# Kernel tuning notes

Measured on AMD Instinct MI355X. Metric: run time of the kernel, lower is better.

## Reference

```python
import jax, jax.numpy as jnp
import numpy as np

DIM = 2048
NUM_LADDERS = 3
DEPTH = 5
EPS = 0.01


def setup_inputs() -> dict:
    key = jax.random.key(0)
    ks = jax.random.split(key, 5)
    s = 1.0 / np.sqrt(DIM)
    x = jax.random.normal(ks[0], (4, 2048, DIM), dtype=jnp.float32)
    U_w = jax.random.uniform(ks[1], (DIM, DIM), jnp.float32, -s, s)          # U.weight  [out,in]
    gate_w = jax.random.uniform(ks[2], (DIM, DIM), jnp.float32, -s, s)       # gate_proj.weight
    ladder_w = jax.random.uniform(ks[3], (NUM_LADDERS, DEPTH + 1, DIM), jnp.float32, -s, s)
    V_w = jax.random.uniform(ks[4], (DIM, NUM_LADDERS), jnp.float32, -1.0 / np.sqrt(NUM_LADDERS), 1.0 / np.sqrt(NUM_LADDERS))
    return {"x": x, "U_w": U_w, "gate_w": gate_w, "ladder_w": ladder_w, "V_w": V_w}


def _continued_fraction(a_cf, eps):
    # a_cf: (..., depth). Evaluate a_1/(1 + a_2/(1 + ... a_d/1)) with
    # epsilon-guarded denominators (pole avoidance).
    d = a_cf.shape[-1]
    f = jnp.zeros(a_cf.shape[:-1], a_cf.dtype)
    for k in reversed(range(d)):  # tiny fixed depth: loop is fine
        denom = 1.0 + f
        denom = jnp.where(jnp.abs(denom) < eps,
                          jnp.where(denom >= 0, eps, -eps), denom)
        f = a_cf[..., k] / denom
    return f


def reference(x, U_w, gate_w, ladder_w, V_w):
    linear_out = jnp.einsum('bsd,od->bso', x, U_w)                 # U(x)
    gated_x = jax.nn.sigmoid(jnp.einsum('bsd,od->bso', x, gate_w)) * x
    # All ladders at once: (b,s,L,depth+1)
    a = jnp.einsum('bsd,lkd->bslk', gated_x, ladder_w)
    a0 = a[..., 0]                                                 # (b,s,L)
    z = a0 + _continued_fraction(a[..., 1:], EPS)                  # (b,s,L)
    combined = jnp.einsum('bsl,dl->bsd', z, V_w)                   # V(z)
    return linear_out + combined
```

## Files before the change

### kernel.cpp

```cpp
#include <hip/hip_runtime.h>
#include <cstdint>
#include <cstddef>

#define DIM 2048
#define NROWS 8192
#define NL 3
#define DEPTH 5
#define NLK 18
#define NCB 16
#define CF_EPS 0.01f

typedef __attribute__((ext_vector_type(8))) __bf16 bfrag;
typedef __attribute__((ext_vector_type(4))) float f32x4;

typedef __attribute__((address_space(1))) void gvoid;
typedef __attribute__((address_space(3))) void lvoid;

__device__ __forceinline__ void gld_lds16(const void* g, void* l) {
    __builtin_amdgcn_global_load_lds((gvoid*)g, (lvoid*)l, 16, 0, 0);
}

__global__ __launch_bounds__(256) void mfma_gemm_u(
    const ushort* __restrict__ A, const ushort* __restrict__ B,
    const float* __restrict__ zb, const float* __restrict__ Vp,
    float* __restrict__ C)
{
    constexpr int BK = 32;
    constexpr int SUB = 128 * BK;
    __shared__ __align__(16) ushort sA[2 * SUB];
    __shared__ __align__(16) ushort sB[2 * SUB];

    const int tid  = threadIdx.x;
    const int wave = tid >> 6;
    const int lane = tid & 63;
    const int wm   = wave & 1;
    const int wn   = wave >> 1;
    const int m0   = blockIdx.y * 128;
    const int n0   = blockIdx.x * 128;

    const size_t soff = (size_t)(wave * 32 + (lane >> 2)) * DIM + (lane & 3) * 8;
    const ushort* gA = A + (size_t)m0 * DIM + soff;
    const ushort* gB = B + (size_t)n0 * DIM + soff;

    ushort* lA0 = &sA[(wave * 32) * BK];
    ushort* lA1 = &sA[(wave * 32 + 16) * BK];
    ushort* lB0 = &sB[(wave * 32) * BK];
    ushort* lB1 = &sB[(wave * 32 + 16) * BK];

    const int fm = lane & 15;
    const int fq = lane >> 4;

    f32x4 acc[4][4];
    #pragma unroll
    for (int i = 0; i < 4; ++i)
        #pragma unroll
        for (int j = 0; j < 4; ++j)
            acc[i][j] = (f32x4){0.f, 0.f, 0.f, 0.f};

    for (int k0 = 0; k0 < DIM; k0 += 2 * BK) {
        __syncthreads();
        gld_lds16(gA + k0, lA0);
        gld_lds16(gA + (size_t)16 * DIM + k0, lA1);
        gld_lds16(gB + k0, lB0);
        gld_lds16(gB + (size_t)16 * DIM + k0, lB1);
        gld_lds16(gA + k0 + BK, lA0 + SUB);
        gld_lds16(gA + (size_t)16 * DIM + k0 + BK, lA1 + SUB);
        gld_lds16(gB + k0 + BK, lB0 + SUB);
        gld_lds16(gB + (size_t)16 * DIM + k0 + BK, lB1 + SUB);
        __syncthreads();

        #pragma unroll
        for (int ks = 0; ks < 2; ++ks) {
            const ushort* pA = &sA[ks * SUB];
            const ushort* pB = &sB[ks * SUB];
            bfrag ah[4], bh[4];
            #pragma unroll
            for (int i = 0; i < 4; ++i) {
                ah[i] = *(const bfrag*)&pA[(wm * 64 + i * 16 + fm) * BK + fq * 8];
                bh[i] = *(const bfrag*)&pB[(wn * 64 + i * 16 + fm) * BK + fq * 8];
            }
            #pragma unroll
            for (int i = 0; i < 4; ++i)
                #pragma unroll
                for (int j = 0; j < 4; ++j)
                    acc[i][j] = __builtin_amdgcn_mfma_f32_16x16x32_bf16(ah[i], bh[j], acc[i][j], 0, 0, 0);
        }
    }

    float4 vc[4];
    #pragma unroll
    for (int j = 0; j < 4; ++j)
        vc[j] = *(const float4*)&Vp[(size_t)(n0 + wn * 64 + j * 16 + fm) * 4];

    #pragma unroll
    for (int i = 0; i < 4; ++i) {
        const int rowb = m0 + wm * 64 + i * 16 + fq * 4;
        #pragma unroll
        for (int r = 0; r < 4; ++r) {
            const float4 zr = *(const float4*)&zb[(size_t)(rowb + r) * 4];
            #pragma unroll
            for (int j = 0; j < 4; ++j) {
                const int col = n0 + wn * 64 + j * 16 + fm;
                C[(size_t)(rowb + r) * DIM + col] =
                    acc[i][j][r] + zr.x * vc[j].x + zr.y * vc[j].y + zr.z * vc[j].z;
            }
        }
    }
}

__global__ __launch_bounds__(256) void mfma_gemm_gate(
    const ushort* __restrict__ Ah, const ushort* __restrict__ Al,
    const ushort* __restrict__ Bh, const ushort* __restrict__ Bl,
    const float* __restrict__ X,  const float* __restrict__ Lw,
    float* __restrict__ a_part)
{
    constexpr int BK = 32;
    __shared__ __align__(16) char smem[32768];
    ushort* sAh = (ushort*)(smem);
    ushort* sBh = (ushort*)(smem + 8192);
    ushort* sAl = (ushort*)(smem + 16384);
    ushort* sBl = (ushort*)(smem + 24576);
    float*  sG  = (float*)(smem);
    float*  sLw = (float*)(smem + 16896);

    const int tid  = threadIdx.x;
    const int wave = tid >> 6;
    const int lane = tid & 63;
    const int wm   = wave & 1;
    const int wn   = wave >> 1;
    const int m0   = blockIdx.y * 128;
    const int n0   = blockIdx.x * 128;

    const size_t soff = (size_t)(wave * 32 + (lane >> 2)) * DIM + (lane & 3) * 8;
    const ushort* gA  = Ah + (size_t)m0 * DIM + soff;
    const ushort* gAl = Al + (size_t)m0 * DIM + soff;
    const ushort* gB  = Bh + (size_t)n0 * DIM + soff;
    const ushort* gBl = Bl + (size_t)n0 * DIM + soff;

    ushort* lA0  = &sAh[(wave * 32) * BK];
    ushort* lA1  = &sAh[(wave * 32 + 16) * BK];
    ushort* lB0  = &sBh[(wave * 32) * BK];
    ushort* lB1  = &sBh[(wave * 32 + 16) * BK];
    ushort* lAl0 = &sAl[(wave * 32) * BK];
    ushort* lAl1 = &sAl[(wave * 32 + 16) * BK];
    ushort* lBl0 = &sBl[(wave * 32) * BK];
    ushort* lBl1 = &sBl[(wave * 32 + 16) * BK];

    const int fm = lane & 15;
    const int fq = lane >> 4;

    f32x4 acc[4][4];
    #pragma unroll
    for (int i = 0; i < 4; ++i)
        #pragma unroll
        for (int j = 0; j < 4; ++j)
            acc[i][j] = (f32x4){0.f, 0.f, 0.f, 0.f};

    for (int k0 = 0; k0 < DIM; k0 += BK) {
        __syncthreads();
        gld_lds16(gA + k0, lA0);
        gld_lds16(gA + (size_t)16 * DIM + k0, lA1);
        gld_lds16(gB + k0, lB0);
        gld_lds16(gB + (size_t)16 * DIM + k0, lB1);
        gld_lds16(gAl + k0, lAl0);
        gld_lds16(gAl + (size_t)16 * DIM + k0, lAl1);
        gld_lds16(gBl + k0, lBl0);
        gld_lds16(gBl + (size_t)16 * DIM + k0, lBl1);
        __syncthreads();

        bfrag ah[4], bh[4], al[4], bl[4];
        #pragma unroll
        for (int i = 0; i < 4; ++i) {
            ah[i] = *(const bfrag*)&sAh[(wm * 64 + i * 16 + fm) * BK + fq * 8];
            bh[i] = *(const bfrag*)&sBh[(wn * 64 + i * 16 + fm) * BK + fq * 8];
            al[i] = *(const bfrag*)&sAl[(wm * 64 + i * 16 + fm) * BK + fq * 8];
            bl[i] = *(const bfrag*)&sBl[(wn * 64 + i * 16 + fm) * BK + fq * 8];
        }
        #pragma unroll
        for (int i = 0; i < 4; ++i)
            #pragma unroll
            for (int j = 0; j < 4; ++j) {
                acc[i][j] = __builtin_amdgcn_mfma_f32_16x16x32_bf16(ah[i], bh[j], acc[i][j], 0, 0, 0);
                acc[i][j] = __builtin_amdgcn_mfma_f32_16x16x32_bf16(ah[i], bl[j], acc[i][j], 0, 0, 0);
                acc[i][j] = __builtin_amdgcn_mfma_f32_16x16x32_bf16(al[i], bh[j], acc[i][j], 0, 0, 0);
            }
    }

    const float* xblk = X + (size_t)m0 * DIM + n0;
    const int rred  = ((tid >> 6) << 3) | (tid & 7);
    const int strip = (lane >> 3) & 7;
    const int qc    = strip * 16;

#define DO_QUARTER(Q)                                                          \
    {                                                                          \
        __syncthreads();     \
        if (Q == 0) {                                                          \
              \
            for (int idx = tid; idx < NLK * 128; idx += 256) {                 \
                const int lk = idx >> 7, c = idx & 127;                        \
                sLw[lk * 156 + c + ((c >> 4) << 2)] = Lw[(size_t)lk * DIM + n0 + c]; \
            }                                                                  \
        }                                                                      \
        if (wm == (Q >> 1)) {                                                  \
            constexpr int ib = (Q & 1) * 2;   \
            _Pragma("unroll")                                                  \
            for (int ii = 0; ii < 2; ++ii) {                                   \
                _Pragma("unroll")                                              \
                for (int r = 0; r < 4; ++r) {                                  \
                    const int rloc = ii * 16 + fq * 4 + r;          \
                    const float* xr = xblk + (size_t)(Q * 32 + rloc) * DIM;    \
                    _Pragma("unroll")                                          \
                    for (int j = 0; j < 4; ++j) {                              \
                        const int cc = wn * 64 + j * 16 + fm;                  \
                        const float g = acc[ib + ii][j][r];                    \
                        const float s = 1.0f / (1.0f + __expf(-g));            \
                        sG[rloc * 132 + cc] = s * xr[cc];                      \
                    }                                                          \
                }                                                              \
            }                                                                  \
        }                                                                      \
        __syncthreads();                         \
        float p[NLK];                                                          \
        _Pragma("unroll")                                                      \
        for (int lk = 0; lk < NLK; ++lk) p[lk] = 0.f;                          \
        _Pragma("unroll")                                                      \
        for (int c4 = 0; c4 < 16; c4 += 4) {                                   \
            const float4 g4 = *(const float4*)&sG[rred * 132 + qc + c4];       \
            _Pragma("unroll")                                                  \
            for (int lk = 0; lk < NLK; ++lk) {                                 \
                const float4 w4 = *(const float4*)&sLw[lk * 156 + qc + c4 + (strip << 2)]; \
                p[lk] = fmaf(g4.x, w4.x, fmaf(g4.y, w4.y,                      \
                        fmaf(g4.z, w4.z, fmaf(g4.w, w4.w, p[lk]))));           \
            }                                                                  \
        }                                                                      \
        _Pragma("unroll")                                                      \
        for (int lk = 0; lk < NLK; ++lk) {                                     \
            p[lk] += __shfl_xor(p[lk], 8, 64);                                 \
            p[lk] += __shfl_xor(p[lk], 16, 64);                                \
            p[lk] += __shfl_xor(p[lk], 32, 64);                                \
        }                                                                      \
        if ((lane >> 3) == 0) {                                                \
            float* dst = a_part +                                              \
                ((size_t)(m0 + Q * 32 + rred) * NCB + blockIdx.x) * NLK;       \
            _Pragma("unroll")                                                  \
            for (int lk = 0; lk < NLK; ++lk) dst[lk] = p[lk];                  \
        }                                                                      \
    }

    DO_QUARTER(0)
    DO_QUARTER(1)
    DO_QUARTER(2)
    DO_QUARTER(3)
#undef DO_QUARTER
}

__global__ __launch_bounds__(256) void cf_kernel(const float* __restrict__ a_part,
                                                 float* __restrict__ zb)
{
    const int r = blockIdx.x * 256 + threadIdx.x;
    const float* ap = a_part + (size_t)r * NCB * NLK;
    float a[NLK];
    #pragma unroll
    for (int lk = 0; lk < NLK; ++lk) a[lk] = 0.f;
    #pragma unroll 4
    for (int cb = 0; cb < NCB; ++cb) {
        #pragma unroll
        for (int lk = 0; lk < NLK; ++lk)
            a[lk] += ap[cb * NLK + lk];
    }
    float z[NL];
    #pragma unroll
    for (int l = 0; l < NL; ++l) {
        float f = 0.f;
        #pragma unroll
        for (int k = DEPTH - 1; k >= 0; --k) {
            float denom = 1.f + f;
            if (fabsf(denom) < CF_EPS) denom = (denom >= 0.f) ? CF_EPS : -CF_EPS;
            f = a[l * (DEPTH + 1) + k + 1] / denom;
        }
        z[l] = a[l * (DEPTH + 1)] + f;
    }
    *(float4*)&zb[(size_t)r * 4] = make_float4(z[0], z[1], z[2], 0.f);
}

__global__ __launch_bounds__(256) void padV(const float* __restrict__ Vw,
                                            float* __restrict__ Vp)
{
    const int d = blockIdx.x * 256 + threadIdx.x;
    *(float4*)&Vp[(size_t)d * 4] =
        make_float4(Vw[(size_t)d * 3], Vw[(size_t)d * 3 + 1], Vw[(size_t)d * 3 + 2], 0.f);
}

__device__ __forceinline__ ushort f2bf_bits(float f) {
    __bf16 h = (__bf16)f;
    return __builtin_bit_cast(unsigned short, h);
}
__device__ __forceinline__ float bfbits2f(ushort u) {
    __bf16 h = __builtin_bit_cast(__bf16, u);
    return (float)h;
}

union U16x8 { ushort u[8]; uint4 v; };

__global__ __launch_bounds__(256) void split2(const float* __restrict__ src,
                                              ushort* __restrict__ hi,
                                              ushort* __restrict__ lo)
{
    const size_t i0 = ((size_t)blockIdx.x * 256 + threadIdx.x) * 8;
    const float4 v0 = *(const float4*)(src + i0);
    const float4 v1 = *(const float4*)(src + i0 + 4);
    const float f[8] = {v0.x, v0.y, v0.z, v0.w, v1.x, v1.y, v1.z, v1.w};
    U16x8 h, l;
    #pragma unroll
    for (int j = 0; j < 8; ++j) {
        const ushort hb = f2bf_bits(f[j]);
        h.u[j] = hb;
        l.u[j] = f2bf_bits(f[j] - bfbits2f(hb));
    }
    *(uint4*)(hi + i0) = h.v;
    *(uint4*)(lo + i0) = l.v;
}

__global__ __launch_bounds__(256) void tobf16(const float* __restrict__ src,
                                              ushort* __restrict__ dst)
{
    const size_t i0 = ((size_t)blockIdx.x * 256 + threadIdx.x) * 8;
    const float4 v0 = *(const float4*)(src + i0);
    const float4 v1 = *(const float4*)(src + i0 + 4);
    const float f[8] = {v0.x, v0.y, v0.z, v0.w, v1.x, v1.y, v1.z, v1.w};
    U16x8 h;
    #pragma unroll
    for (int j = 0; j < 8; ++j) h.u[j] = f2bf_bits(f[j]);
    *(uint4*)(dst + i0) = h.v;
}

#define BMF 128
#define BNF 128
#define BKF 16
#define LDAF 132

__global__ __launch_bounds__(256) void sgemm_dual(
    const float* __restrict__ X,
    const float* __restrict__ Uw,
    const float* __restrict__ Gw,
    float* __restrict__ outLin,
    float* __restrict__ outGate)
{
    __shared__ float As[BKF][LDAF];
    __shared__ float Bs[BKF][LDAF];

    const int tid = threadIdx.x;
    const int n0 = blockIdx.x * BNF;
    const int m0 = blockIdx.y * BMF;
    const bool isGate = (n0 >= DIM);
    const float* W = isGate ? Gw : Uw;
    float* C = isGate ? outGate : outLin;
    const int nb = isGate ? (n0 - DIM) : n0;

    const int lr = tid >> 2;
    const int lc = (tid & 3) << 2;

    const float* pa0 = X + (size_t)(m0 + lr) * DIM + lc;
    const float* pa1 = X + (size_t)(m0 + lr + 64) * DIM + lc;
    const float* pb0 = W + (size_t)(nb + lr) * DIM + lc;
    const float* pb1 = W + (size_t)(nb + lr + 64) * DIM + lc;

    const int tx = tid & 15;
    const int ty = tid >> 4;

    float acc[8][8];
    #pragma unroll
    for (int i = 0; i < 8; ++i)
        #pragma unroll
        for (int j = 0; j < 8; ++j) acc[i][j] = 0.f;

    for (int k0 = 0; k0 < DIM; k0 += BKF) {
        const float4 a0 = *(const float4*)(pa0 + k0);
        const float4 a1 = *(const float4*)(pa1 + k0);
        const float4 b0 = *(const float4*)(pb0 + k0);
        const float4 b1 = *(const float4*)(pb1 + k0);
        __syncthreads();
        As[lc + 0][lr] = a0.x; As[lc + 1][lr] = a0.y; As[lc + 2][lr] = a0.z; As[lc + 3][lr] = a0.w;
        As[lc + 0][lr + 64] = a1.x; As[lc + 1][lr + 64] = a1.y; As[lc + 2][lr + 64] = a1.z; As[lc + 3][lr + 64] = a1.w;
        Bs[lc + 0][lr] = b0.x; Bs[lc + 1][lr] = b0.y; Bs[lc + 2][lr] = b0.z; Bs[lc + 3][lr] = b0.w;
        Bs[lc + 0][lr + 64] = b1.x; Bs[lc + 1][lr + 64] = b1.y; Bs[lc + 2][lr + 64] = b1.z; Bs[lc + 3][lr + 64] = b1.w;
        __syncthreads();
        #pragma unroll
        for (int kk = 0; kk < BKF; ++kk) {
            float av[8], bv[8];
            *(float4*)&av[0] = *(const float4*)&As[kk][ty * 8];
            *(float4*)&av[4] = *(const float4*)&As[kk][ty * 8 + 4];
            *(float4*)&bv[0] = *(const float4*)&Bs[kk][tx * 8];
            *(float4*)&bv[4] = *(const float4*)&Bs[kk][tx * 8 + 4];
            #pragma unroll
            for (int i = 0; i < 8; ++i)
                #pragma unroll
                for (int j = 0; j < 8; ++j)
                    acc[i][j] = fmaf(av[i], bv[j], acc[i][j]);
        }
    }

    #pragma unroll
    for (int i = 0; i < 8; ++i) {
        float* crow = C + (size_t)(m0 + ty * 8 + i) * DIM + nb + tx * 8;
        *(float4*)crow       = make_float4(acc[i][0], acc[i][1], acc[i][2], acc[i][3]);
        *(float4*)(crow + 4) = make_float4(acc[i][4], acc[i][5], acc[i][6], acc[i][7]);
    }
}

__global__ __launch_bounds__(256) void ladder_epilogue(
    const float* __restrict__ X,
    const float* __restrict__ G,
    const float* __restrict__ Lw,
    const float* __restrict__ Vw,
    float* __restrict__ Out)
{
    const int r = blockIdx.x;
    const int tid = threadIdx.x;
    const int d0 = tid * 8;
    const float* xrow = X + (size_t)r * DIM;
    const float* grow = G + (size_t)r * DIM;

    const float4 xv0 = *(const float4*)(xrow + d0);
    const float4 xv1 = *(const float4*)(xrow + d0 + 4);
    const float4 gv0 = *(const float4*)(grow + d0);
    const float4 gv1 = *(const float4*)(grow + d0 + 4);

    float gated[8];
    {
        const float gx[8] = {gv0.x, gv0.y, gv0.z, gv0.w, gv1.x, gv1.y, gv1.z, gv1.w};
        const float xx[8] = {xv0.x, xv0.y, xv0.z, xv0.w, xv1.x, xv1.y, xv1.z, xv1.w};
        #pragma unroll
        for (int j = 0; j < 8; ++j) {
            const float s = 1.0f / (1.0f + __expf(-gx[j]));
            gated[j] = s * xx[j];
        }
    }

    float part[NLK];
    #pragma unroll
    for (int lk = 0; lk < NLK; ++lk) {
        const float* lrow = Lw + (size_t)lk * DIM + d0;
        const float4 w0 = *(const float4*)lrow;
        const float4 w1 = *(const float4*)(lrow + 4);
        part[lk] = gated[0] * w0.x + gated[1] * w0.y + gated[2] * w0.z + gated[3] * w0.w
                 + gated[4] * w1.x + gated[5] * w1.y + gated[6] * w1.z + gated[7] * w1.w;
    }

    #pragma unroll
    for (int off = 32; off > 0; off >>= 1) {
        #pragma unroll
        for (int lk = 0; lk < NLK; ++lk)
            part[lk] += __shfl_down(part[lk], off, 64);
    }

    __shared__ float red[4][NLK];
    __shared__ float zsh[NL];
    const int wave = tid >> 6;
    const int lane = tid & 63;
    if (lane == 0) {
        #pragma unroll
        for (int lk = 0; lk < NLK; ++lk) red[wave][lk] = part[lk];
    }
    __syncthreads();
    if (tid < NL) {
        float a[DEPTH + 1];
        #pragma unroll
        for (int k = 0; k < DEPTH + 1; ++k)
            a[k] = red[0][tid * 6 + k] + red[1][tid * 6 + k]
                 + red[2][tid * 6 + k] + red[3][tid * 6 + k];
        float f = 0.f;
        #pragma unroll
        for (int k = DEPTH - 1; k >= 0; --k) {
            float denom = 1.f + f;
            if (fabsf(denom) < CF_EPS) denom = (denom >= 0.f) ? CF_EPS : -CF_EPS;
            f = a[k + 1] / denom;
        }
        zsh[tid] = a[0] + f;
    }
    __syncthreads();
    const float z0 = zsh[0], z1 = zsh[1], z2 = zsh[2];

    float* orow = Out + (size_t)r * DIM + d0;
    const float4 o0 = *(const float4*)orow;
    const float4 o1 = *(const float4*)(orow + 4);
    float ov[8] = {o0.x, o0.y, o0.z, o0.w, o1.x, o1.y, o1.z, o1.w};
    #pragma unroll
    for (int j = 0; j < 8; ++j) {
        const float* vp = Vw + (size_t)(d0 + j) * NL;
        ov[j] += z0 * vp[0] + z1 * vp[1] + z2 * vp[2];
    }
    *(float4*)orow       = make_float4(ov[0], ov[1], ov[2], ov[3]);
    *(float4*)(orow + 4) = make_float4(ov[4], ov[5], ov[6], ov[7]);
}

extern "C" void kernel_launch(void* const* d_in, const int* in_sizes, int n_in,
                              void* d_out, int out_size, void* d_ws, size_t ws_size,
                              hipStream_t stream) {
    const float* X  = (const float*)d_in[0];
    const float* Uw = (const float*)d_in[1];
    const float* Gw = (const float*)d_in[2];
    const float* Lw = (const float*)d_in[3];
    const float* Vw = (const float*)d_in[4];
    float* out = (float*)d_out;

    const size_t WS_NEED = 101875712ull;
    char* ws = (char*)d_ws;

    if (ws_size >= WS_NEED) {
        ushort* Xh     = (ushort*)(ws);
        ushort* Xl     = (ushort*)(ws + 33554432);
        ushort* Gwh    = (ushort*)(ws + 67108864);
        ushort* Gwl    = (ushort*)(ws + 75497472);
        ushort* Uwh    = (ushort*)(ws + 83886080);
        float*  a_part = (float*)(ws + 92274688);
        float*  z_buf  = (float*)(ws + 101711872);
        float*  Vp     = (float*)(ws + 101842944);

        split2<<<dim3(8192), dim3(256), 0, stream>>>(X, Xh, Xl);
        split2<<<dim3(2048), dim3(256), 0, stream>>>(Gw, Gwh, Gwl);
        tobf16<<<dim3(2048), dim3(256), 0, stream>>>(Uw, Uwh);
        padV  <<<dim3(8),    dim3(256), 0, stream>>>(Vw, Vp);

        dim3 grid(DIM / 128, NROWS / 128);
        mfma_gemm_gate<<<grid, dim3(256), 0, stream>>>(Xh, Xl, Gwh, Gwl, X, Lw, a_part);
        cf_kernel<<<dim3(32), dim3(256), 0, stream>>>(a_part, z_buf);
        mfma_gemm_u<<<grid, dim3(256), 0, stream>>>(Xh, Uwh, z_buf, Vp, out);
    } else {
        float* gbuf = (float*)ws;
        dim3 grid(2 * DIM / BNF, NROWS / BMF);
        sgemm_dual<<<grid, dim3(256), 0, stream>>>(X, Uw, Gw, out, gbuf);
        ladder_epilogue<<<dim3(NROWS), dim3(256), 0, stream>>>(X, gbuf, Lw, Vw, out);
    }
}
```

Baseline: 485.6 us.

## Merge gate and U GEMMs into one launch; apply CF and V in a final row pass

The gate GEMM (with its ladder epilogue) and the U GEMM now run as one kernel, with odd and even block columns selecting which GEMM each block computes. This lets both run concurrently and cuts a launch plus the serialization between them. The continued-fraction reduction and the V(z) rank-3 update move into a new per-row kernel that reads back the full output, adds z·V, and writes it again. That costs an extra read and write of the 64MB output, and the interleaved blocks have unequal work, since gate blocks do split-precision loads while U blocks do a single bf16 pass.

```diff
diff --git a/kernel.cpp b/kernel.cpp
--- a/kernel.cpp
+++ b/kernel.cpp
@@ -20,102 +20,95 @@
     __builtin_amdgcn_global_load_lds((gvoid*)g, (lvoid*)l, 16, 0, 0);
 }
 
-__global__ __launch_bounds__(256) void mfma_gemm_u(
-    const ushort* __restrict__ A, const ushort* __restrict__ B,
-    const float* __restrict__ zb, const float* __restrict__ Vp,
-    float* __restrict__ C)
+__global__ __launch_bounds__(256) void gemm_mixed(
+    const ushort* __restrict__ Xh, const ushort* __restrict__ Xl,
+    const ushort* __restrict__ Gwh, const ushort* __restrict__ Gwl,
+    const ushort* __restrict__ Uwh,
+    const float* __restrict__ X,  const float* __restrict__ Lw,
+    float* __restrict__ outU, float* __restrict__ a_part)
 {
     constexpr int BK = 32;
-    constexpr int SUB = 128 * BK;
-    __shared__ __align__(16) ushort sA[2 * SUB];
-    __shared__ __align__(16) ushort sB[2 * SUB];
+    __shared__ __align__(16) char smem[32768];
 
     const int tid  = threadIdx.x;
     const int wave = tid >> 6;
     const int lane = tid & 63;
     const int wm   = wave & 1;
     const int wn   = wave >> 1;
+    const int bx   = blockIdx.x;
+    const int cb   = bx >> 1;
     const int m0   = blockIdx.y * 128;
-    const int n0   = blockIdx.x * 128;
-
-    const size_t soff = (size_t)(wave * 32 + (lane >> 2)) * DIM + (lane & 3) * 8;
-    const ushort* gA = A + (size_t)m0 * DIM + soff;
-    const ushort* gB = B + (size_t)n0 * DIM + soff;
-
-    ushort* lA0 = &sA[(wave * 32) * BK];
-    ushort* lA1 = &sA[(wave * 32 + 16) * BK];
-    ushort* lB0 = &sB[(wave * 32) * BK];
-    ushort* lB1 = &sB[(wave * 32 + 16) * BK];
+    const int n0   = cb * 128;
 
     const int fm = lane & 15;
     const int fq = lane >> 4;
 
-    f32x4 acc[4][4];
-    #pragma unroll
-    for (int i = 0; i < 4; ++i)
-        #pragma unroll
-        for (int j = 0; j < 4; ++j)
-            acc[i][j] = (f32x4){0.f, 0.f, 0.f, 0.f};
-
-    for (int k0 = 0; k0 < DIM; k0 += 2 * BK) {
-        __syncthreads();
-        gld_lds16(gA + k0, lA0);
-        gld_lds16(gA + (size_t)16 * DIM + k0, lA1);
-        gld_lds16(gB + k0, lB0);
-        gld_lds16(gB + (size_t)16 * DIM + k0, lB1);
-        gld_lds16(gA + k0 + BK, lA0 + SUB);
-        gld_lds16(gA + (size_t)16 * DIM + k0 + BK, lA1 + SUB);
-        gld_lds16(gB + k0 + BK, lB0 + SUB);
-        gld_lds16(gB + (size_t)16 * DIM + k0 + BK, lB1 + SUB);
-        __syncthreads();
-
-        #pragma unroll
-        for (int ks = 0; ks < 2; ++ks) {
-            const ushort* pA = &sA[ks * SUB];
-            const ushort* pB = &sB[ks * SUB];
-            bfrag ah[4], bh[4];
+    const size_t soff = (size_t)(wave * 32 + (lane >> 2)) * DIM + (lane & 3) * 8;
+
+    if (bx & 1) {
+        constexpr int SUB = 128 * BK;
+        ushort* sA = (ushort*)smem;
+        ushort* sB = (ushort*)(smem + 16384);
+
+        const ushort* gA = Xh  + (size_t)m0 * DIM + soff;
+        const ushort* gB = Uwh + (size_t)n0 * DIM + soff;
+
+        ushort* lA0 = &sA[(wave * 32) * BK];
+        ushort* lA1 = &sA[(wave * 32 + 16) * BK];
+        ushort* lB0 = &sB[(wave * 32) * BK];
+        ushort* lB1 = &sB[(wave * 32 + 16) * BK];
+
+        f32x4 acc[4][4];
+        #pragma unroll
+        for (int i = 0; i < 4; ++i)
             #pragma unroll
-            for (int i = 0; i < 4; ++i) {
-                ah[i] = *(const bfrag*)&pA[(wm * 64 + i * 16 + fm) * BK + fq * 8];
-                bh[i] = *(const bfrag*)&pB[(wn * 64 + i * 16 + fm) * BK + fq * 8];
+            for (int j = 0; j < 4; ++j)
+                acc[i][j] = (f32x4){0.f, 0.f, 0.f, 0.f};
+
+        for (int k0 = 0; k0 < DIM; k0 += 2 * BK) {
+            __syncthreads();
+            gld_lds16(gA + k0, lA0);
+            gld_lds16(gA + (size_t)16 * DIM + k0, lA1);
+            gld_lds16(gB + k0, lB0);
+            gld_lds16(gB + (size_t)16 * DIM + k0, lB1);
+            gld_lds16(gA + k0 + BK, lA0 + SUB);
+            gld_lds16(gA + (size_t)16 * DIM + k0 + BK, lA1 + SUB);
+            gld_lds16(gB + k0 + BK, lB0 + SUB);
+            gld_lds16(gB + (size_t)16 * DIM + k0 + BK, lB1 + SUB);
+            __syncthreads();
+
+            #pragma unroll
+            for (int ks = 0; ks < 2; ++ks) {
+                const ushort* pA = &sA[ks * SUB];
+                const ushort* pB = &sB[ks * SUB];
+                bfrag ah[4], bh[4];
+                #pragma unroll
+                for (int i = 0; i < 4; ++i) {
+                    ah[i] = *(const bfrag*)&pA[(wm * 64 + i * 16 + fm) * BK + fq * 8];
+                    bh[i] = *(const bfrag*)&pB[(wn * 64 + i * 16 + fm) * BK + fq * 8];
+                }
+                #pragma unroll
+                for (int i = 0; i < 4; ++i)
+                    #pragma unroll
+                    for (int j = 0; j < 4; ++j)
+                        acc[i][j] = __builtin_amdgcn_mfma_f32_16x16x32_bf16(ah[i], bh[j], acc[i][j], 0, 0, 0);
             }
-            #pragma unroll
-            for (int i = 0; i < 4; ++i)
-                #pragma unroll
-                for (int j = 0; j < 4; ++j)
-                    acc[i][j] = __builtin_amdgcn_mfma_f32_16x16x32_bf16(ah[i], bh[j], acc[i][j], 0, 0, 0);
-        }
-    }
-
-    float4 vc[4];
-    #pragma unroll
-    for (int j = 0; j < 4; ++j)
-        vc[j] = *(const float4*)&Vp[(size_t)(n0 + wn * 64 + j * 16 + fm) * 4];
-
-    #pragma unroll
-    for (int i = 0; i < 4; ++i) {
-        const int rowb = m0 + wm * 64 + i * 16 + fq * 4;
-        #pragma unroll
-        for (int r = 0; r < 4; ++r) {
-            const float4 zr = *(const float4*)&zb[(size_t)(rowb + r) * 4];
+        }
+
+        #pragma unroll
+        for (int i = 0; i < 4; ++i) {
+            const int rowb = m0 + wm * 64 + i * 16 + fq * 4;
             #pragma unroll
             for (int j = 0; j < 4; ++j) {
                 const int col = n0 + wn * 64 + j * 16 + fm;
-                C[(size_t)(rowb + r) * DIM + col] =
-                    acc[i][j][r] + zr.x * vc[j].x + zr.y * vc[j].y + zr.z * vc[j].z;
+                #pragma unroll
+                for (int r = 0; r < 4; ++r)
+                    outU[(size_t)(rowb + r) * DIM + col] = acc[i][j][r];
             }
         }
-    }
-}
-
-__global__ __launch_bounds__(256) void mfma_gemm_gate(
-    const ushort* __restrict__ Ah, const ushort* __restrict__ Al,
-    const ushort* __restrict__ Bh, const ushort* __restrict__ Bl,
-    const float* __restrict__ X,  const float* __restrict__ Lw,
-    float* __restrict__ a_part)
-{
-    constexpr int BK = 32;
-    __shared__ __align__(16) char smem[32768];
+        return;
+    }
+
     ushort* sAh = (ushort*)(smem);
     ushort* sBh = (ushort*)(smem + 8192);
     ushort* sAl = (ushort*)(smem + 16384);
@@ -123,19 +116,10 @@
     float*  sG  = (float*)(smem);
     float*  sLw = (float*)(smem + 16896);
 
-    const int tid  = threadIdx.x;
-    const int wave = tid >> 6;
-    const int lane = tid & 63;
-    const int wm   = wave & 1;
-    const int wn   = wave >> 1;
-    const int m0   = blockIdx.y * 128;
-    const int n0   = blockIdx.x * 128;
-
-    const size_t soff = (size_t)(wave * 32 + (lane >> 2)) * DIM + (lane & 3) * 8;
-    const ushort* gA  = Ah + (size_t)m0 * DIM + soff;
-    const ushort* gAl = Al + (size_t)m0 * DIM + soff;
-    const ushort* gB  = Bh + (size_t)n0 * DIM + soff;
-    const ushort* gBl = Bl + (size_t)n0 * DIM + soff;
+    const ushort* gA  = Xh  + (size_t)m0 * DIM + soff;
+    const ushort* gAl = Xl  + (size_t)m0 * DIM + soff;
+    const ushort* gB  = Gwh + (size_t)n0 * DIM + soff;
+    const ushort* gBl = Gwl + (size_t)n0 * DIM + soff;
 
     ushort* lA0  = &sAh[(wave * 32) * BK];
     ushort* lA1  = &sAh[(wave * 32 + 16) * BK];
@@ -145,9 +129,6 @@
     ushort* lAl1 = &sAl[(wave * 32 + 16) * BK];
     ushort* lBl0 = &sBl[(wave * 32) * BK];
     ushort* lBl1 = &sBl[(wave * 32 + 16) * BK];
-
-    const int fm = lane & 15;
-    const int fq = lane >> 4;
 
     f32x4 acc[4][4];
     #pragma unroll
@@ -241,7 +222,7 @@
         }                                                                      \
         if ((lane >> 3) == 0) {                                                \
             float* dst = a_part +                                              \
-                ((size_t)(m0 + Q * 32 + rred) * NCB + blockIdx.x) * NLK;       \
+                ((size_t)(m0 + Q * 32 + rred) * NCB + cb) * NLK;               \
             _Pragma("unroll")                                                  \
             for (int lk = 0; lk < NLK; ++lk) dst[lk] = p[lk];                  \
         }                                                                      \
@@ -254,33 +235,48 @@
 #undef DO_QUARTER
 }
 
-__global__ __launch_bounds__(256) void cf_kernel(const float* __restrict__ a_part,
-                                                 float* __restrict__ zb)
-{
-    const int r = blockIdx.x * 256 + threadIdx.x;
-    const float* ap = a_part + (size_t)r * NCB * NLK;
-    float a[NLK];
-    #pragma unroll
-    for (int lk = 0; lk < NLK; ++lk) a[lk] = 0.f;
-    #pragma unroll 4
-    for (int cb = 0; cb < NCB; ++cb) {
-        #pragma unroll
-        for (int lk = 0; lk < NLK; ++lk)
-            a[lk] += ap[cb * NLK + lk];
-    }
-    float z[NL];
-    #pragma unroll
-    for (int l = 0; l < NL; ++l) {
+__global__ __launch_bounds__(256) void zv_cf_add(
+    float* __restrict__ out, const float* __restrict__ a_part,
+    const float* __restrict__ Vp)
+{
+    __shared__ float red[NLK];
+    __shared__ float zsh[NL];
+    const int r = blockIdx.x;
+    const int tid = threadIdx.x;
+
+    if (tid < NLK) {
+        const float* ap = a_part + (size_t)r * NCB * NLK + tid;
+        float s = 0.f;
+        #pragma unroll
+        for (int cb = 0; cb < NCB; ++cb) s += ap[cb * NLK];
+        red[tid] = s;
+    }
+    __syncthreads();
+    if (tid < NL) {
         float f = 0.f;
         #pragma unroll
         for (int k = DEPTH - 1; k >= 0; --k) {
             float denom = 1.f + f;
             if (fabsf(denom) < CF_EPS) denom = (denom >= 0.f) ? CF_EPS : -CF_EPS;
-            f = a[l * (DEPTH + 1) + k + 1] / denom;
-        }
-        z[l] = a[l * (DEPTH + 1)] + f;
-    }
-    *(float4*)&zb[(size_t)r * 4] = make_float4(z[0], z[1], z[2], 0.f);
+            f = red[tid * 6 + k + 1] / denom;
+        }
+        zsh[tid] = red[tid * 6] + f;
+    }
+    __syncthreads();
+    const float z0 = zsh[0], z1 = zsh[1], z2 = zsh[2];
+
+    const int c0 = tid * 8;
+    float* orow = out + (size_t)r * DIM + c0;
+    const float4 o0 = *(const float4*)orow;
+    const float4 o1 = *(const float4*)(orow + 4);
+    float ov[8] = {o0.x, o0.y, o0.z, o0.w, o1.x, o1.y, o1.z, o1.w};
+    #pragma unroll
+    for (int j = 0; j < 8; ++j) {
+        const float4 v = *(const float4*)&Vp[(size_t)(c0 + j) * 4];
+        ov[j] += z0 * v.x + z1 * v.y + z2 * v.z;
+    }
+    *(float4*)orow       = make_float4(ov[0], ov[1], ov[2], ov[3]);
+    *(float4*)(orow + 4) = make_float4(ov[4], ov[5], ov[6], ov[7]);
 }
 
 __global__ __launch_bounds__(256) void padV(const float* __restrict__ Vw,
@@ -504,7 +500,7 @@
     const float* Vw = (const float*)d_in[4];
     float* out = (float*)d_out;
 
-    const size_t WS_NEED = 101875712ull;
+    const size_t WS_NEED = 101744640ull;
     char* ws = (char*)d_ws;
 
     if (ws_size >= WS_NEED) {
@@ -514,18 +510,16 @@
         ushort* Gwl    = (ushort*)(ws + 75497472);
         ushort* Uwh    = (ushort*)(ws + 83886080);
         float*  a_part = (float*)(ws + 92274688);
-        float*  z_buf  = (float*)(ws + 101711872);
-        float*  Vp     = (float*)(ws + 101842944);
+        float*  Vp     = (float*)(ws + 101711872);
 
         split2<<<dim3(8192), dim3(256), 0, stream>>>(X, Xh, Xl);
         split2<<<dim3(2048), dim3(256), 0, stream>>>(Gw, Gwh, Gwl);
         tobf16<<<dim3(2048), dim3(256), 0, stream>>>(Uw, Uwh);
         padV  <<<dim3(8),    dim3(256), 0, stream>>>(Vw, Vp);
 
-        dim3 grid(DIM / 128, NROWS / 128);
-        mfma_gemm_gate<<<grid, dim3(256), 0, stream>>>(Xh, Xl, Gwh, Gwl, X, Lw, a_part);
-        cf_kernel<<<dim3(32), dim3(256), 0, stream>>>(a_part, z_buf);
-        mfma_gemm_u<<<grid, dim3(256), 0, stream>>>(Xh, Uwh, z_buf, Vp, out);
+        gemm_mixed<<<dim3(32, 64), dim3(256), 0, stream>>>(Xh, Xl, Gwh, Gwl, Uwh,
+                                                           X, Lw, out, a_part);
+        zv_cf_add<<<dim3(NROWS), dim3(256), 0, stream>>>(out, a_part, Vp);
     } else {
         float* gbuf = (float*)ws;
         dim3 grid(2 * DIM / BNF, NROWS / BMF);
```

After: 620.4 us. +27.8%, slower.
